# Optimization experiments

Measured on AMD Instinct MI355X. Metric: run time of the kernel, lower is better.

The kernel has to match this reference:

```python
import jax, jax.numpy as jnp
import numpy as np


def setup_inputs() -> dict:
    key = jax.random.key(0)
    k1, k2 = jax.random.split(key)
    B, F = 512, 1024
    K, D = 100, 5
    inputs = jax.random.normal(k1, (B, F), dtype=jnp.float32)
    T = jax.random.normal(k2, (F, K * D), dtype=jnp.float32) * 0.05  # random_normal init
    return {"inputs": inputs, "T": T}


def reference(inputs, T):
    NUM_KERNELS, DIM_PER_KERNEL = 100, 5
    B = inputs.shape[0]
    # project: [B, F] @ [F, K*D] -> [B, K, D]
    x = (inputs @ T).reshape(B, NUM_KERNELS, DIM_PER_KERNEL)
    # pairwise L1 over D: abs_diffs[i, k, j] = sum_d |x[i,k,d] - x[j,k,d]|
    # diffs: [B, K, D, B]
    diffs = x[:, :, :, None] - jnp.transpose(x, (1, 2, 0))[None, :, :, :]
    abs_diffs = jnp.sum(jnp.abs(diffs), axis=2)  # [B, K, B]
    # sum over other-batch axis (includes self term exp(0)=1, as in original)
    minibatch_features = jnp.sum(jnp.exp(-abs_diffs), axis=2)  # [B, K]
    return minibatch_features
```

## Files before the change

kernel.cpp:

```cpp
#include <hip/hip_runtime.h>


#define BB 512
#define FF 1024
#define KK 100
#define KD 500
#define KDP 512
#define SPLITS 8
#define FN (FF / SPLITS)
#define STEPS (FN / 16)
#define LOG2E 1.4426950408889634f

__global__ __launch_bounds__(256, 2) void kA(
    const float* __restrict__ in, const float* __restrict__ T,
    float* __restrict__ xpT)
{
    __shared__ __align__(16) float smem[2112];
    float (*Ads)[68] = (float(*)[68])smem;
    float (*Bds)[64] = (float(*)[64])(smem + 1088);

    const int b = blockIdx.x;
    const int t = threadIdx.x;
    const int i0  = (b & 7) * 64;
    const int kd0 = ((b >> 3) & 7) * 64;
    const int s   = b >> 6;
    const int tk  = t & 15;
    const int ti  = t >> 4;

    float acc[4][4];
    #pragma unroll
    for (int r = 0; r < 4; ++r)
        #pragma unroll
        for (int c = 0; c < 4; ++c) acc[r][c] = 0.f;

    const int ia  = t >> 2;
    const int fqa = t & 3;
    const int kb  = t & 63;
    const int frb = t >> 6;
    const int kbc = min(kd0 + kb, KD - 1);

    const float* inb = in + (size_t)(i0 + ia) * FF + s * FN;
    const float* Tb  = T + (size_t)(s * FN) * KD + kbc;

    float4 av = *(const float4*)&inb[fqa * 4];
    float bv0 = Tb[(size_t)(frb * 4 + 0) * KD];
    float bv1 = Tb[(size_t)(frb * 4 + 1) * KD];
    float bv2 = Tb[(size_t)(frb * 4 + 2) * KD];
    float bv3 = Tb[(size_t)(frb * 4 + 3) * KD];

    for (int step = 0; step < STEPS; ++step) {
        Ads[fqa * 4 + 0][ia] = av.x;
        Ads[fqa * 4 + 1][ia] = av.y;
        Ads[fqa * 4 + 2][ia] = av.z;
        Ads[fqa * 4 + 3][ia] = av.w;
        Bds[frb * 4 + 0][kb] = bv0;
        Bds[frb * 4 + 1][kb] = bv1;
        Bds[frb * 4 + 2][kb] = bv2;
        Bds[frb * 4 + 3][kb] = bv3;
        __syncthreads();

        if (step + 1 < STEPS) {
            const int fo = (step + 1) * 16;
            av  = *(const float4*)&inb[fo + fqa * 4];
            bv0 = Tb[(size_t)(fo + frb * 4 + 0) * KD];
            bv1 = Tb[(size_t)(fo + frb * 4 + 1) * KD];
            bv2 = Tb[(size_t)(fo + frb * 4 + 2) * KD];
            bv3 = Tb[(size_t)(fo + frb * 4 + 3) * KD];
        }

        #pragma unroll
        for (int f = 0; f < 16; ++f) {
            float4 a  = *(const float4*)&Ads[f][ti * 4];
            float4 bq = *(const float4*)&Bds[f][tk * 4];
            float ar[4] = {a.x, a.y, a.z, a.w};
            float br[4] = {bq.x, bq.y, bq.z, bq.w};
            #pragma unroll
            for (int r = 0; r < 4; ++r)
                #pragma unroll
                for (int c = 0; c < 4; ++c)
                    acc[r][c] = fmaf(ar[r], br[c], acc[r][c]);
        }
        __syncthreads();
    }

    #pragma unroll
    for (int c = 0; c < 4; ++c) {
        float4 v = {acc[0][c], acc[1][c], acc[2][c], acc[3][c]};
        *(float4*)&xpT[((size_t)s * KDP + kd0 + tk * 4 + c) * BB + i0 + ti * 4] = v;
    }
}

__global__ __launch_bounds__(256) void kB(
    const float* __restrict__ xpT, float* __restrict__ xT)
{
    const int e = blockIdx.x * 256 + threadIdx.x;
    const float4* p = (const float4*)xpT;
    float4 v = p[e];
    #pragma unroll
    for (int s = 1; s < SPLITS; ++s) {
        float4 w = p[(size_t)s * (KDP * BB / 4) + e];
        v.x += w.x; v.y += w.y; v.z += w.z; v.w += w.w;
    }
    v.x *= LOG2E; v.y *= LOG2E; v.z *= LOG2E; v.w *= LOG2E;
    ((float4*)xT)[e] = v;
}

__global__ __launch_bounds__(256) void pairZ(
    const float* __restrict__ xT, float* __restrict__ out)
{
    const int k  = blockIdx.x;
    const int ip = blockIdx.y;
    const int jp = blockIdx.z;
    const int t  = threadIdx.x;
    const int lane = t & 63;
    const int w    = t >> 6;

    __shared__ float xs4[128][4];
    __shared__ float xs1[128];
    __shared__ float ps[4][128];

    for (int e = t; e < 640; e += 256) {
        const int d  = e >> 7;
        const int jj = e & 127;
        const float v = xT[(size_t)(k * 5 + d) * BB + jp * 128 + jj];
        if (d < 4) xs4[jj][d] = v; else xs1[jj] = v;
    }
    __syncthreads();

    float xa[5], xb[5];
    #pragma unroll
    for (int d = 0; d < 5; ++d) {
        xa[d] = xT[(size_t)(k * 5 + d) * BB + ip * 128 + lane];
        xb[d] = xT[(size_t)(k * 5 + d) * BB + ip * 128 + 64 + lane];
    }

    float sa0 = 0.f, sa1 = 0.f, sb0 = 0.f, sb1 = 0.f;
    const int j0 = w << 5;
    #pragma unroll 2
    for (int jj = 0; jj < 32; jj += 2) {
        {
            const int j = j0 + jj;
            float4 xj = *(const float4*)&xs4[j][0];
            float  x4 = xs1[j];
            float aa = (fabsf(xa[0] - xj.x) + fabsf(xa[1] - xj.y))
                     + (fabsf(xa[2] - xj.z) + fabsf(xa[3] - xj.w))
                     + fabsf(xa[4] - x4);
            float bb = (fabsf(xb[0] - xj.x) + fabsf(xb[1] - xj.y))
                     + (fabsf(xb[2] - xj.z) + fabsf(xb[3] - xj.w))
                     + fabsf(xb[4] - x4);
            sa0 += __builtin_amdgcn_exp2f(-aa);
            sb0 += __builtin_amdgcn_exp2f(-bb);
        }
        {
            const int j = j0 + jj + 1;
            float4 xj = *(const float4*)&xs4[j][0];
            float  x4 = xs1[j];
            float aa = (fabsf(xa[0] - xj.x) + fabsf(xa[1] - xj.y))
                     + (fabsf(xa[2] - xj.z) + fabsf(xa[3] - xj.w))
                     + fabsf(xa[4] - x4);
            float bb = (fabsf(xb[0] - xj.x) + fabsf(xb[1] - xj.y))
                     + (fabsf(xb[2] - xj.z) + fabsf(xb[3] - xj.w))
                     + fabsf(xb[4] - x4);
            sa1 += __builtin_amdgcn_exp2f(-aa);
            sb1 += __builtin_amdgcn_exp2f(-bb);
        }
    }

    ps[w][lane]      = sa0 + sa1;
    ps[w][lane + 64] = sb0 + sb1;
    __syncthreads();

    if (t < 128) {
        const float v = (ps[0][t] + ps[1][t]) + (ps[2][t] + ps[3][t]);
        unsafeAtomicAdd(&out[(size_t)(ip * 128 + t) * KK + k], v);
    }
}

__global__ __launch_bounds__(1024, 1) void mbd_fused(
    const float* __restrict__ in, const float* __restrict__ T, float* __restrict__ out)
{
    const int k = blockIdx.x;
    const int t = threadIdx.x;
    const int i = t & (BB - 1);
    const int h = t >> 9;

    __shared__ float xk[1024][8];

    float a0 = 0.f, a1 = 0.f, a2 = 0.f, a3 = 0.f, a4 = 0.f;
    const float4* inrow = (const float4*)(in + (size_t)i * FF + (size_t)h * 512);
    const float* Tk = T + 5 * k + (size_t)h * 512 * KD;

    for (int ff = 0; ff < 512; ff += 4) {
        float4 v = inrow[ff >> 2];
        const float* tp = Tk + (size_t)ff * KD;
        a0 = fmaf(v.x, tp[0], a0); a1 = fmaf(v.x, tp[1], a1); a2 = fmaf(v.x, tp[2], a2);
        a3 = fmaf(v.x, tp[3], a3); a4 = fmaf(v.x, tp[4], a4); tp += KD;
        a0 = fmaf(v.y, tp[0], a0); a1 = fmaf(v.y, tp[1], a1); a2 = fmaf(v.y, tp[2], a2);
        a3 = fmaf(v.y, tp[3], a3); a4 = fmaf(v.y, tp[4], a4); tp += KD;
        a0 = fmaf(v.z, tp[0], a0); a1 = fmaf(v.z, tp[1], a1); a2 = fmaf(v.z, tp[2], a2);
        a3 = fmaf(v.z, tp[3], a3); a4 = fmaf(v.z, tp[4], a4); tp += KD;
        a0 = fmaf(v.w, tp[0], a0); a1 = fmaf(v.w, tp[1], a1); a2 = fmaf(v.w, tp[2], a2);
        a3 = fmaf(v.w, tp[3], a3); a4 = fmaf(v.w, tp[4], a4);
    }
    xk[t][0] = a0; xk[t][1] = a1; xk[t][2] = a2; xk[t][3] = a3; xk[t][4] = a4;
    __syncthreads();
    if (t < BB) {
        xk[t][0] += xk[t + BB][0]; xk[t][1] += xk[t + BB][1]; xk[t][2] += xk[t + BB][2];
        xk[t][3] += xk[t + BB][3]; xk[t][4] += xk[t + BB][4];
    }
    __syncthreads();

    const int jg = t >> 9;
    const float4 xiv = *(const float4*)&xk[i][0];
    const float xi4 = xk[i][4];
    float s0 = 0.f;
    const int j0 = jg << 8;
    for (int jj = 0; jj < 256; ++jj) {
        const int j = j0 + jj;
        float4 xj = *(const float4*)&xk[j][0];
        float xj4 = xk[j][4];
        float aa = (fabsf(xiv.x - xj.x) + fabsf(xiv.y - xj.y))
                 + (fabsf(xiv.z - xj.z) + fabsf(xiv.w - xj.w)) + fabsf(xi4 - xj4);
        s0 += __builtin_amdgcn_exp2f(-1.4426950408889634f * aa);
    }
    xk[BB + i][jg] = s0;
    __syncthreads();
    if (t < BB)
        out[(size_t)t * KK + k] = xk[BB + t][0] + xk[BB + t][1];
}

extern "C" void kernel_launch(void* const* d_in, const int* in_sizes, int n_in,
                              void* d_out, int out_size, void* d_ws, size_t ws_size,
                              hipStream_t stream) {
    const float* in = (const float*)d_in[0];
    const float* T  = (const float*)d_in[1];
    float* out = (float*)d_out;

    const size_t xpT_bytes = (size_t)SPLITS * KDP * BB * sizeof(float);
    const size_t xT_bytes  = (size_t)KDP * BB * sizeof(float);

    if (ws_size < xpT_bytes + xT_bytes) {
        mbd_fused<<<KK, 1024, 0, stream>>>(in, T, out);
        return;
    }

    float* xpT = (float*)d_ws;
    float* xT  = (float*)((char*)d_ws + xpT_bytes);

    hipMemsetAsync(out, 0, (size_t)BB * KK * sizeof(float), stream);

    kA<<<512, 256, 0, stream>>>(in, T, xpT);
    kB<<<256, 256, 0, stream>>>(xpT, xT);

    dim3 g3(KK, 4, 4);
    pairZ<<<g3, 256, 0, stream>>>(xT, out);
}
```

Measured before the change: 40.83 us.

## Retile pairwise kernel so each thread covers eight i rows over a 64-wide j slice

```diff
diff --git a/kernel.cpp b/kernel.cpp
--- a/kernel.cpp
+++ b/kernel.cpp
@@ -105,74 +105,67 @@
     ((float4*)xT)[e] = v;
 }
 
-__global__ __launch_bounds__(256) void pairZ(
+__global__ __launch_bounds__(256) void pair8(
     const float* __restrict__ xT, float* __restrict__ out)
 {
     const int k  = blockIdx.x;
-    const int ip = blockIdx.y;
-    const int jp = blockIdx.z;
+    const int jp = blockIdx.y;
     const int t  = threadIdx.x;
     const int lane = t & 63;
     const int w    = t >> 6;
 
-    __shared__ float xs4[128][4];
-    __shared__ float xs1[128];
-    __shared__ float ps[4][128];
-
-    for (int e = t; e < 640; e += 256) {
-        const int d  = e >> 7;
-        const int jj = e & 127;
-        const float v = xT[(size_t)(k * 5 + d) * BB + jp * 128 + jj];
-        if (d < 4) xs4[jj][d] = v; else xs1[jj] = v;
-    }
-    __syncthreads();
-
-    float xa[5], xb[5];
-    #pragma unroll
-    for (int d = 0; d < 5; ++d) {
-        xa[d] = xT[(size_t)(k * 5 + d) * BB + ip * 128 + lane];
-        xb[d] = xT[(size_t)(k * 5 + d) * BB + ip * 128 + 64 + lane];
-    }
-
-    float sa0 = 0.f, sa1 = 0.f, sb0 = 0.f, sb1 = 0.f;
-    const int j0 = w << 5;
+    __shared__ float xs4[BB][4];
+    __shared__ float xs1[BB];
+    __shared__ float ps[4][BB];
+
+    #pragma unroll
+    for (int q = 0; q < 2; ++q) {
+        const int j = t + q * 256;
+        float d0 = xT[(size_t)(k * 5 + 0) * BB + j];
+        float d1 = xT[(size_t)(k * 5 + 1) * BB + j];
+        float d2 = xT[(size_t)(k * 5 + 2) * BB + j];
+        float d3 = xT[(size_t)(k * 5 + 3) * BB + j];
+        float d4 = xT[(size_t)(k * 5 + 4) * BB + j];
+        float4 v = {d0, d1, d2, d3};
+        *(float4*)&xs4[j][0] = v;
+        xs1[j] = d4;
+    }
+    __syncthreads();
+
+    float xi[8][5];
+    #pragma unroll
+    for (int r = 0; r < 8; ++r) {
+        const int i = r * 64 + lane;
+        float4 v = *(const float4*)&xs4[i][0];
+        xi[r][0] = v.x; xi[r][1] = v.y; xi[r][2] = v.z; xi[r][3] = v.w;
+        xi[r][4] = xs1[i];
+    }
+
+    float acc[8] = {0.f, 0.f, 0.f, 0.f, 0.f, 0.f, 0.f, 0.f};
+    const int j0 = jp * 64 + w * 16;
     #pragma unroll 2
-    for (int jj = 0; jj < 32; jj += 2) {
-        {
-            const int j = j0 + jj;
-            float4 xj = *(const float4*)&xs4[j][0];
-            float  x4 = xs1[j];
-            float aa = (fabsf(xa[0] - xj.x) + fabsf(xa[1] - xj.y))
-                     + (fabsf(xa[2] - xj.z) + fabsf(xa[3] - xj.w))
-                     + fabsf(xa[4] - x4);
-            float bb = (fabsf(xb[0] - xj.x) + fabsf(xb[1] - xj.y))
-                     + (fabsf(xb[2] - xj.z) + fabsf(xb[3] - xj.w))
-                     + fabsf(xb[4] - x4);
-            sa0 += __builtin_amdgcn_exp2f(-aa);
-            sb0 += __builtin_amdgcn_exp2f(-bb);
+    for (int jj = 0; jj < 16; ++jj) {
+        const int j = j0 + jj;
+        float4 xj = *(const float4*)&xs4[j][0];
+        float  x4 = xs1[j];
+        #pragma unroll
+        for (int r = 0; r < 8; ++r) {
+            float aa = (fabsf(xi[r][0] - xj.x) + fabsf(xi[r][1] - xj.y))
+                     + (fabsf(xi[r][2] - xj.z) + fabsf(xi[r][3] - xj.w))
+                     + fabsf(xi[r][4] - x4);
+            acc[r] += __builtin_amdgcn_exp2f(-aa);
         }
-        {
-            const int j = j0 + jj + 1;
-            float4 xj = *(const float4*)&xs4[j][0];
-            float  x4 = xs1[j];
-            float aa = (fabsf(xa[0] - xj.x) + fabsf(xa[1] - xj.y))
-                     + (fabsf(xa[2] - xj.z) + fabsf(xa[3] - xj.w))
-                     + fabsf(xa[4] - x4);
-            float bb = (fabsf(xb[0] - xj.x) + fabsf(xb[1] - xj.y))
-                     + (fabsf(xb[2] - xj.z) + fabsf(xb[3] - xj.w))
-                     + fabsf(xb[4] - x4);
-            sa1 += __builtin_amdgcn_exp2f(-aa);
-            sb1 += __builtin_amdgcn_exp2f(-bb);
-        }
-    }
-
-    ps[w][lane]      = sa0 + sa1;
-    ps[w][lane + 64] = sb0 + sb1;
-    __syncthreads();
-
-    if (t < 128) {
-        const float v = (ps[0][t] + ps[1][t]) + (ps[2][t] + ps[3][t]);
-        unsafeAtomicAdd(&out[(size_t)(ip * 128 + t) * KK + k], v);
+    }
+
+    #pragma unroll
+    for (int r = 0; r < 8; ++r) ps[w][r * 64 + lane] = acc[r];
+    __syncthreads();
+
+    #pragma unroll
+    for (int q = 0; q < 2; ++q) {
+        const int i = t + q * 256;
+        const float v = (ps[0][i] + ps[1][i]) + (ps[2][i] + ps[3][i]);
+        unsafeAtomicAdd(&out[(size_t)i * KK + k], v);
     }
 }
 
@@ -252,6 +245,6 @@
     kA<<<512, 256, 0, stream>>>(in, T, xpT);
     kB<<<256, 256, 0, stream>>>(xpT, xT);
 
-    dim3 g3(KK, 4, 4);
-    pairZ<<<g3, 256, 0, stream>>>(xT, out);
-}
+    dim3 g3(KK, 8);
+    pair8<<<g3, 256, 0, stream>>>(xT, out);
+}
```

New measurement: 53.76 us. 1.32x slower.
